# Kernel tuning notes

Hardware: AMD Instinct MI355X
Metric: run time of the kernel (lower is better)

## Reference

```python
import jax, jax.numpy as jnp
import numpy as np

N = 50000   # num_nodes
E = 1600000 # edges (avg degree 32)
D = 256     # in_feats
H = 256     # n_hidden


def setup_inputs() -> dict:
    key = jax.random.key(0)
    ks = jax.random.split(key, 9)
    s = 1.0 / np.sqrt(D)
    return {
        "input_nodes": jnp.arange(N, dtype=jnp.int32),
        "edge_src": jax.random.randint(ks[0], (E,), 0, N, dtype=jnp.int32),
        "edge_dst": jax.random.randint(ks[1], (E,), 0, N, dtype=jnp.int32),
        "emb": jax.random.normal(ks[2], (N, D), jnp.float32) * 0.02,
        "W_self0": jax.random.normal(ks[3], (D, H), jnp.float32) * s,
        "W_neigh0": jax.random.normal(ks[4], (D, H), jnp.float32) * s,
        "b0": jnp.zeros((H,), jnp.float32),
        "W_self1": jax.random.normal(ks[5], (H, H), jnp.float32) * s,
        "W_neigh1": jax.random.normal(ks[6], (H, H), jnp.float32) * s,
        "b1": jnp.zeros((H,), jnp.float32),
    }


def _sage_mean(h, src, dst, W_self, W_neigh, b, n):
    # gather neighbor features, mean-reduce by destination, then linear.
    msgs = h[src]                                                  # [E, d]
    ssum = jax.ops.segment_sum(msgs, dst, num_segments=n)          # [n, d]
    deg = jax.ops.segment_sum(jnp.ones(src.shape, h.dtype), dst, num_segments=n)
    h_neigh = ssum / jnp.maximum(deg, 1.0)[:, None]
    return h @ W_self + h_neigh @ W_neigh + b


def reference(input_nodes, edge_src, edge_dst, emb,
              W_self0, W_neigh0, b0, W_self1, W_neigh1, b1):
    h = emb[input_nodes]                                            # [N, D]
    h = _sage_mean(h, edge_src, edge_dst, W_self0, W_neigh0, b0, N)
    h = jax.nn.relu(h)  # dropout is identity at inference
    h = _sage_mean(h, edge_src, edge_dst, W_self1, W_neigh1, b1, N)
    h = h / jnp.linalg.norm(h)  # global Frobenius norm, as in torch.norm(h)
    return h
```

## Files before the change

### kernel.cpp

```cpp
#include <hip/hip_runtime.h>
#include <math.h>

#define NN 50000
#define NE 1600000
#define DF 256
#define NBUCK 391

typedef unsigned short ushortT;
typedef __attribute__((ext_vector_type(8))) short short8;
typedef __attribute__((ext_vector_type(4))) float floatx4;

__device__ __forceinline__ unsigned bf16rne(float f) {
    unsigned u = __float_as_uint(f);
    return (u + 0x7fffu + ((u >> 16) & 1u)) >> 16;
}

#define ASYNC16(gptr, ldsptr) \
    __builtin_amdgcn_global_load_lds((const __attribute__((address_space(1))) unsigned*)(gptr), \
                                     (__attribute__((address_space(3))) unsigned*)(ldsptr), 16, 0, 0)


__global__ void k_zero(int* __restrict__ bcnt) {
    int i = blockIdx.x * 256 + threadIdx.x;
    if (i < NBUCK) bcnt[i] = 0;
}

__global__ __launch_bounds__(256)
void k_bhist(const int* __restrict__ dst, int* __restrict__ bcnt) {
    __shared__ int h[NBUCK];
    for (int i = threadIdx.x; i < NBUCK; i += 256) h[i] = 0;
    __syncthreads();
    int base = blockIdx.x * 4096;
#pragma unroll
    for (int i = 0; i < 16; ++i) {
        int e = base + i * 256 + threadIdx.x;
        if (e < NE) atomicAdd(&h[dst[e] >> 7], 1);
    }
    __syncthreads();
    for (int i = threadIdx.x; i < NBUCK; i += 256)
        if (h[i]) atomicAdd(&bcnt[i], h[i]);
}

__global__ void k_bscan(const int* __restrict__ bcnt, int* __restrict__ bbase,
                        int* __restrict__ cursor, int* __restrict__ row_ptr,
                        float* __restrict__ nrm) {
    __shared__ int s[512];
    int t = threadIdx.x;
    int v = (t < NBUCK) ? bcnt[t] : 0;
    s[t] = v; __syncthreads();
    for (int off = 1; off < 512; off <<= 1) {
        int x = (t >= off) ? s[t - off] : 0;
        __syncthreads();
        s[t] += x;
        __syncthreads();
    }
    if (t < NBUCK) { bbase[t] = s[t] - v; cursor[t] = s[t] - v; }
    if (t == 0) { bbase[NBUCK] = NE; row_ptr[NN] = NE; *nrm = 0.0f; }
}

__global__ __launch_bounds__(256)
void k_bin(const int* __restrict__ src, const int* __restrict__ dst,
           int* __restrict__ cursor, unsigned* __restrict__ rec) {
    __shared__ int h[NBUCK];
    __shared__ int gb[NBUCK];
    for (int i = threadIdx.x; i < NBUCK; i += 256) h[i] = 0;
    __syncthreads();
    const int base = blockIdx.x * 2048;
    int bk[8], rk[8];
    unsigned pk[8];
#pragma unroll
    for (int i = 0; i < 8; ++i) {
        int e = base + i * 256 + threadIdx.x;
        if (e < NE) {
            int d = dst[e];
            bk[i] = d >> 7;
            pk[i] = (unsigned)src[e] | ((unsigned)(d & 127) << 16);
            rk[i] = atomicAdd(&h[bk[i]], 1);
        } else bk[i] = -1;
    }
    __syncthreads();
    for (int i = threadIdx.x; i < NBUCK; i += 256) {
        int c = h[i];
        gb[i] = c ? atomicAdd(&cursor[i], c) : 0;
    }
    __syncthreads();
#pragma unroll
    for (int i = 0; i < 8; ++i)
        if (bk[i] >= 0) rec[gb[bk[i]] + rk[i]] = pk[i];
}

__global__ __launch_bounds__(256)
void k_csr(const unsigned* __restrict__ rec, const int* __restrict__ bbase,
           int* __restrict__ row_ptr, ushortT* __restrict__ csr) {
    __shared__ int cnt[128];
    __shared__ int cur[128];
    __shared__ int s[256];
    const int B = blockIdx.x, t = threadIdx.x;
    if (t < 128) cnt[t] = 0;
    __syncthreads();
    const int beg = bbase[B], end = bbase[B + 1];
    for (int p = beg + t; p < end; p += 256)
        atomicAdd(&cnt[(rec[p] >> 16) & 127], 1);
    __syncthreads();
    int v = (t < 128) ? cnt[t] : 0;
    s[t] = v; __syncthreads();
    for (int off = 1; off < 256; off <<= 1) {
        int x = (t >= off) ? s[t - off] : 0;
        __syncthreads();
        s[t] += x;
        __syncthreads();
    }
    if (t < 128) {
        int ex = s[t] - v;
        cur[t] = ex;
        int node = B * 128 + t;
        if (node < NN) row_ptr[node] = beg + ex;
    }
    __syncthreads();
    for (int p = beg + t; p < end; p += 256) {
        unsigned r = rec[p];
        int loc = atomicAdd(&cur[(r >> 16) & 127], 1);
        csr[beg + loc] = (ushortT)r;
    }
}


__global__ __launch_bounds__(256)
void k_cvt(const float* __restrict__ emb, const int* __restrict__ gather,
           ushortT* __restrict__ embb,
           const float* __restrict__ Ws0, const float* __restrict__ Wn0,
           ushortT* __restrict__ Wt0,
           const float* __restrict__ Ws1, const float* __restrict__ Wn1,
           ushortT* __restrict__ Wt1) {
    const int b = blockIdx.x;
    if (b < 6250) {
        long long i = ((long long)b * 256 + threadIdx.x) * 8;
        int row = (int)(i >> 8);
        int col = (int)(i & 255);
        long long g = (long long)gather[row] * 256 + col;
        float4 v0 = *(const float4*)(emb + g);
        float4 v1 = *(const float4*)(emb + g + 4);
        uint4 o;
        o.x = bf16rne(v0.x) | (bf16rne(v0.y) << 16);
        o.y = bf16rne(v0.z) | (bf16rne(v0.w) << 16);
        o.z = bf16rne(v1.x) | (bf16rne(v1.y) << 16);
        o.w = bf16rne(v1.z) | (bf16rne(v1.w) << 16);
        *(uint4*)(embb + i) = o;
    } else {
        const bool first = b < 6762;
        const int idx = ((first ? b - 6250 : b - 6762)) * 256 + threadIdx.x;
        const int n = idx >> 9;
        const int k = idx & 511;
        const float* Ws = first ? Ws0 : Ws1;
        const float* Wn = first ? Wn0 : Wn1;
        float v = (k < 256) ? Ws[k * 256 + n] : Wn[(k - 256) * 256 + n];
        (first ? Wt0 : Wt1)[idx] = (ushortT)bf16rne(v);
    }
}


__global__ __launch_bounds__(256)
void k_agg(const ushortT* __restrict__ feat, const int* __restrict__ row_ptr,
           const ushortT* __restrict__ csr, ushortT* __restrict__ out) {
    int node = blockIdx.x * 4 + (threadIdx.x >> 6);
    int lane = threadIdx.x & 63;
    int half = lane >> 5;
    int l5 = lane & 31;
    if (node >= NN) return;
    int beg = row_ptr[node], end = row_ptr[node + 1];

    float s[8] = {0.f, 0.f, 0.f, 0.f, 0.f, 0.f, 0.f, 0.f};
    int p = beg + half;

#define ACCUM(q) do { \
        s[0] += __uint_as_float(q.x << 16); \
        s[1] += __uint_as_float(q.x & 0xffff0000u); \
        s[2] += __uint_as_float(q.y << 16); \
        s[3] += __uint_as_float(q.y & 0xffff0000u); \
        s[4] += __uint_as_float(q.z << 16); \
        s[5] += __uint_as_float(q.z & 0xffff0000u); \
        s[6] += __uint_as_float(q.w << 16); \
        s[7] += __uint_as_float(q.w & 0xffff0000u); \
    } while (0)

    for (; p + 6 < end; p += 8) {
        int r0 = (int)csr[p]     * DF + l5 * 8;
        int r1 = (int)csr[p + 2] * DF + l5 * 8;
        int r2 = (int)csr[p + 4] * DF + l5 * 8;
        int r3 = (int)csr[p + 6] * DF + l5 * 8;
        uint4 a = *(const uint4*)(feat + r0);
        uint4 b = *(const uint4*)(feat + r1);
        uint4 c = *(const uint4*)(feat + r2);
        uint4 d = *(const uint4*)(feat + r3);
        ACCUM(a); ACCUM(b); ACCUM(c); ACCUM(d);
    }
    for (; p < end; p += 2) {
        int r0 = (int)csr[p] * DF + l5 * 8;
        uint4 a = *(const uint4*)(feat + r0);
        ACCUM(a);
    }
#undef ACCUM

#pragma unroll
    for (int k = 0; k < 8; ++k) s[k] += __shfl_down(s[k], 32);

    if (half == 0) {
        float inv = 1.0f / fmaxf((float)(end - beg), 1.0f);
        uint4 o;
        o.x = bf16rne(s[0] * inv) | (bf16rne(s[1] * inv) << 16);
        o.y = bf16rne(s[2] * inv) | (bf16rne(s[3] * inv) << 16);
        o.z = bf16rne(s[4] * inv) | (bf16rne(s[5] * inv) << 16);
        o.w = bf16rne(s[6] * inv) | (bf16rne(s[7] * inv) << 16);
        *(uint4*)(out + (long long)node * DF + l5 * 8) = o;
    }
}


template<int RELU, int NORM>
__global__ __launch_bounds__(256, 4)
void k_gemm(const ushortT* __restrict__ Aself, const ushortT* __restrict__ Aneigh,
            const ushortT* __restrict__ Wt, const float* __restrict__ bias,
            ushortT* __restrict__ Cb, float* __restrict__ Cf, float* __restrict__ norm_acc) {
    __shared__ ushortT As[2048];
    __shared__ ushortT Bs[8192];
    __shared__ float red[4];

    const int t = threadIdx.x;
    const int w = t >> 6;
    const int lane = t & 63;
    const int m0 = blockIdx.x * 64;

    const int ar = t >> 2;
    const int cu = (t & 3) * 8;

    const long long gA = (long long)min(m0 + ar, NN - 1) * 256;

    const unsigned ldsA = w * 512;
    const unsigned ldsB = w * 512;

    const int fm = lane & 15;
    const int fk = (lane >> 4) * 8;

    floatx4 acc[4][4];
#pragma unroll
    for (int i = 0; i < 4; ++i)
#pragma unroll
        for (int j = 0; j < 4; ++j) acc[i][j] = (floatx4){0.f, 0.f, 0.f, 0.f};

    for (int kt = 0; kt < 512; kt += 32) {
        const ushortT* Ab; int kc;
        if (kt < 256) { Ab = Aself; kc = kt; } else { Ab = Aneigh; kc = kt - 256; }

        __syncthreads();
        ASYNC16(Ab + gA + kc + cu, As + ldsA);
#pragma unroll
        for (int i = 0; i < 4; ++i)
            ASYNC16(Wt + (i * 64 + ar) * 512 + kt + cu, Bs + i * 2048 + ldsB);
        __syncthreads();

        short8 af[4], bf[4];
#pragma unroll
        for (int i = 0; i < 4; ++i)
            af[i] = *(const short8*)&As[(i * 16 + fm) * 32 + fk];
#pragma unroll
        for (int j = 0; j < 4; ++j)
            bf[j] = *(const short8*)&Bs[(w * 64 + j * 16 + fm) * 32 + fk];
#pragma unroll
        for (int i = 0; i < 4; ++i)
#pragma unroll
            for (int j = 0; j < 4; ++j)
                acc[i][j] = __builtin_amdgcn_mfma_f32_16x16x32_bf16(af[i], bf[j], acc[i][j], 0, 0, 0);
    }

    float bj[4];
#pragma unroll
    for (int j = 0; j < 4; ++j) bj[j] = bias[w * 64 + j * 16 + fm];

    float sumsq = 0.0f;
#pragma unroll
    for (int i = 0; i < 4; ++i) {
#pragma unroll
        for (int r = 0; r < 4; ++r) {
            const int row = m0 + i * 16 + (lane >> 4) * 4 + r;
            if (row < NN) {
#pragma unroll
                for (int j = 0; j < 4; ++j) {
                    const int col = w * 64 + j * 16 + fm;
                    float v = acc[i][j][r] + bj[j];
                    if (RELU) v = fmaxf(v, 0.0f);
                    if (NORM) {
                        Cf[(long long)row * 256 + col] = v;
                        sumsq += v * v;
                    } else {
                        Cb[(long long)row * 256 + col] = (ushortT)bf16rne(v);
                    }
                }
            }
        }
    }

    if (NORM) {
#pragma unroll
        for (int off = 32; off > 0; off >>= 1) sumsq += __shfl_down(sumsq, off);
        if (lane == 0) red[w] = sumsq;
        __syncthreads();
        if (t == 0) atomicAdd(norm_acc, red[0] + red[1] + red[2] + red[3]);
    }
}

__global__ void k_scale(float* __restrict__ out, const float* __restrict__ nrm) {
    const float s = 1.0f / sqrtf(*nrm);
    long long i = ((long long)blockIdx.x * 256 + threadIdx.x) * 4;
    float4 v = *(float4*)&out[i];
    v.x *= s; v.y *= s; v.z *= s; v.w *= s;
    *(float4*)&out[i] = v;
}


extern "C" void kernel_launch(void* const* d_in, const int* in_sizes, int n_in,
                              void* d_out, int out_size, void* d_ws, size_t ws_size,
                              hipStream_t stream) {
    const int*   input_nodes = (const int*)d_in[0];
    const int*   esrc = (const int*)d_in[1];
    const int*   edst = (const int*)d_in[2];
    const float* emb  = (const float*)d_in[3];
    const float* Ws0  = (const float*)d_in[4];
    const float* Wn0  = (const float*)d_in[5];
    const float* b0   = (const float*)d_in[6];
    const float* Ws1  = (const float*)d_in[7];
    const float* Wn1  = (const float*)d_in[8];
    const float* b1   = (const float*)d_in[9];
    float* out = (float*)d_out;

    char* base = (char*)d_ws;
    ushortT*  embb    = (ushortT*) (base);
    ushortT*  h1b     = (ushortT*) (base + 25600000);
    ushortT*  hnb     = (ushortT*) (base + 51200000);
    unsigned* rec     = (unsigned*)(base + 76800000);
    ushortT*  csr     = (ushortT*) (base + 83200000);
    ushortT*  Wt0     = (ushortT*) (base + 86400000);
    ushortT*  Wt1     = (ushortT*) (base + 86662144);
    int*      row_ptr = (int*)     (base + 86924288);
    int*      bcnt    = (int*)     (base + 87124304);
    int*      bbase   = (int*)     (base + 87125904);
    int*      cursor  = (int*)     (base + 87127504);
    float*    nrm     = (float*)   (base + 87129104);

    k_zero  <<<2,     256, 0, stream>>>(bcnt);
    k_bhist <<<391,   256, 0, stream>>>(edst, bcnt);
    k_bscan <<<1,     512, 0, stream>>>(bcnt, bbase, cursor, row_ptr, nrm);
    k_bin   <<<782,   256, 0, stream>>>(esrc, edst, cursor, rec);
    k_csr   <<<NBUCK, 256, 0, stream>>>(rec, bbase, row_ptr, csr);

    k_cvt<<<7274, 256, 0, stream>>>(emb, input_nodes, embb, Ws0, Wn0, Wt0, Ws1, Wn1, Wt1);

    const int GEMM_BLOCKS = (NN + 63) / 64;

    k_agg<<<NN / 4, 256, 0, stream>>>(embb, row_ptr, csr, hnb);
    k_gemm<1, 0><<<GEMM_BLOCKS, 256, 0, stream>>>(embb, hnb, Wt0, b0, h1b, nullptr, nullptr);

    k_agg<<<NN / 4, 256, 0, stream>>>(h1b, row_ptr, csr, hnb);
    k_gemm<0, 1><<<GEMM_BLOCKS, 256, 0, stream>>>(h1b, hnb, Wt1, b1, nullptr, out, nrm);

    k_scale<<<NN * DF / 4 / 256, 256, 0, stream>>>(out, nrm);
}
```

Baseline: 473.6 us.

## Store bf16 features in 32-column chunked layout for cache-friendly gather

Bf16 node features switch from row-major [N,256] to eight column chunks of [N,32]. The aggregation kernel now gives each block one chunk, and each lane handles 8 columns of one of 16 edges in flight. This shrinks the working set of each gather pass so it fits better in cache. The GEMM A loads and the layer-1 output store are rewritten for the new layout. In exchange, each edge index is re-read eight times, the grid is eight times larger, the GEMM writes scattered 2-byte values, and the CSR loads and output stores use nontemporal hints.

```diff
diff --git a/kernel.cpp b/kernel.cpp
--- a/kernel.cpp
+++ b/kernel.cpp
@@ -5,10 +5,12 @@
 #define NE 1600000
 #define DF 256
 #define NBUCK 391
+#define CHS ((long long)NN * 32)
 
 typedef unsigned short ushortT;
 typedef __attribute__((ext_vector_type(8))) short short8;
 typedef __attribute__((ext_vector_type(4))) float floatx4;
+typedef __attribute__((ext_vector_type(4))) unsigned uintx4;
 
 __device__ __forceinline__ unsigned bf16rne(float f) {
     unsigned u = __float_as_uint(f);
@@ -145,7 +147,7 @@
         o.y = bf16rne(v0.z) | (bf16rne(v0.w) << 16);
         o.z = bf16rne(v1.x) | (bf16rne(v1.y) << 16);
         o.w = bf16rne(v1.z) | (bf16rne(v1.w) << 16);
-        *(uint4*)(embb + i) = o;
+        *(uint4*)(embb + ((long long)(col >> 5) * NN + row) * 32 + (col & 31)) = o;
     } else {
         const bool first = b < 6762;
         const int idx = ((first ? b - 6250 : b - 6762)) * 256 + threadIdx.x;
@@ -162,15 +164,19 @@
 __global__ __launch_bounds__(256)
 void k_agg(const ushortT* __restrict__ feat, const int* __restrict__ row_ptr,
            const ushortT* __restrict__ csr, ushortT* __restrict__ out) {
-    int node = blockIdx.x * 4 + (threadIdx.x >> 6);
-    int lane = threadIdx.x & 63;
-    int half = lane >> 5;
-    int l5 = lane & 31;
+    const int c    = blockIdx.x & 7;
+    const int ng   = blockIdx.x >> 3;
+    const int w    = threadIdx.x >> 6;
+    const int lane = threadIdx.x & 63;
+    const int node = ng * 4 + w;
     if (node >= NN) return;
-    int beg = row_ptr[node], end = row_ptr[node + 1];
+
+    const ushortT* fc = feat + (long long)c * CHS;
+    const int beg = row_ptr[node], end = row_ptr[node + 1];
+    const int eo   = lane >> 2;
+    const int part = (lane & 3) * 8;
 
     float s[8] = {0.f, 0.f, 0.f, 0.f, 0.f, 0.f, 0.f, 0.f};
-    int p = beg + half;
 
 #define ACCUM(q) do { \
         s[0] += __uint_as_float(q.x << 16); \
@@ -183,35 +189,29 @@
         s[7] += __uint_as_float(q.w & 0xffff0000u); \
     } while (0)
 
-    for (; p + 6 < end; p += 8) {
-        int r0 = (int)csr[p]     * DF + l5 * 8;
-        int r1 = (int)csr[p + 2] * DF + l5 * 8;
-        int r2 = (int)csr[p + 4] * DF + l5 * 8;
-        int r3 = (int)csr[p + 6] * DF + l5 * 8;
-        uint4 a = *(const uint4*)(feat + r0);
-        uint4 b = *(const uint4*)(feat + r1);
-        uint4 c = *(const uint4*)(feat + r2);
-        uint4 d = *(const uint4*)(feat + r3);
-        ACCUM(a); ACCUM(b); ACCUM(c); ACCUM(d);
-    }
-    for (; p < end; p += 2) {
-        int r0 = (int)csr[p] * DF + l5 * 8;
-        uint4 a = *(const uint4*)(feat + r0);
-        ACCUM(a);
+    for (int p = beg + eo; p < end; p += 16) {
+        int sidx = (int)__builtin_nontemporal_load(csr + p);
+        uintx4 q = *(const uintx4*)(fc + sidx * 32 + part);
+        ACCUM(q);
     }
 #undef ACCUM
 
 #pragma unroll
-    for (int k = 0; k < 8; ++k) s[k] += __shfl_down(s[k], 32);
-
-    if (half == 0) {
+    for (int k = 0; k < 8; ++k) {
+        s[k] += __shfl_xor(s[k], 4);
+        s[k] += __shfl_xor(s[k], 8);
+        s[k] += __shfl_xor(s[k], 16);
+        s[k] += __shfl_xor(s[k], 32);
+    }
+
+    if (lane < 4) {
         float inv = 1.0f / fmaxf((float)(end - beg), 1.0f);
-        uint4 o;
+        uintx4 o;
         o.x = bf16rne(s[0] * inv) | (bf16rne(s[1] * inv) << 16);
         o.y = bf16rne(s[2] * inv) | (bf16rne(s[3] * inv) << 16);
         o.z = bf16rne(s[4] * inv) | (bf16rne(s[5] * inv) << 16);
         o.w = bf16rne(s[6] * inv) | (bf16rne(s[7] * inv) << 16);
-        *(uint4*)(out + (long long)node * DF + l5 * 8) = o;
+        __builtin_nontemporal_store(o, (uintx4*)(out + ((long long)c * NN + node) * 32 + part));
     }
 }
 
@@ -233,7 +233,7 @@
     const int ar = t >> 2;
     const int cu = (t & 3) * 8;
 
-    const long long gA = (long long)min(m0 + ar, NN - 1) * 256;
+    const long long gA = (long long)min(m0 + ar, NN - 1) * 32 + cu;
 
     const unsigned ldsA = w * 512;
     const unsigned ldsB = w * 512;
@@ -248,11 +248,12 @@
         for (int j = 0; j < 4; ++j) acc[i][j] = (floatx4){0.f, 0.f, 0.f, 0.f};
 
     for (int kt = 0; kt < 512; kt += 32) {
-        const ushortT* Ab; int kc;
-        if (kt < 256) { Ab = Aself; kc = kt; } else { Ab = Aneigh; kc = kt - 256; }
-
-        __syncthreads();
-        ASYNC16(Ab + gA + kc + cu, As + ldsA);
+        const ushortT* Ab = (kt < 256)
+            ? (Aself  + (long long)(kt >> 5) * CHS)
+            : (Aneigh + (long long)((kt - 256) >> 5) * CHS);
+
+        __syncthreads();
+        ASYNC16(Ab + gA, As + ldsA);
 #pragma unroll
         for (int i = 0; i < 4; ++i)
             ASYNC16(Wt + (i * 64 + ar) * 512 + kt + cu, Bs + i * 2048 + ldsB);
@@ -292,7 +293,7 @@
                         Cf[(long long)row * 256 + col] = v;
                         sumsq += v * v;
                     } else {
-                        Cb[(long long)row * 256 + col] = (ushortT)bf16rne(v);
+                        Cb[((long long)(col >> 5) * NN + row) * 32 + (col & 31)] = (ushortT)bf16rne(v);
                     }
                 }
             }
@@ -355,11 +356,12 @@
     k_cvt<<<7274, 256, 0, stream>>>(emb, input_nodes, embb, Ws0, Wn0, Wt0, Ws1, Wn1, Wt1);
 
     const int GEMM_BLOCKS = (NN + 63) / 64;
-
-    k_agg<<<NN / 4, 256, 0, stream>>>(embb, row_ptr, csr, hnb);
+    const int AGG_BLOCKS  = (NN / 4) * 8;
+
+    k_agg<<<AGG_BLOCKS, 256, 0, stream>>>(embb, row_ptr, csr, hnb);
     k_gemm<1, 0><<<GEMM_BLOCKS, 256, 0, stream>>>(embb, hnb, Wt0, b0, h1b, nullptr, nullptr);
 
-    k_agg<<<NN / 4, 256, 0, stream>>>(h1b, row_ptr, csr, hnb);
+    k_agg<<<AGG_BLOCKS, 256, 0, stream>>>(h1b, row_ptr, csr, hnb);
     k_gemm<0, 1><<<GEMM_BLOCKS, 256, 0, stream>>>(h1b, hnb, Wt1, b1, nullptr, out, nrm);
 
     k_scale<<<NN * DF / 4 / 256, 256, 0, stream>>>(out, nrm);
```

Result: slower. 610.9 us (+29.0%).
